# Kernel tuning notes

Measured on AMD Instinct MI355X. Metric: run time of the kernel, lower is better.

## Reference

```python
import jax, jax.numpy as jnp
import numpy as np
from jax import lax

EPS = 1e-5


def _binary(x):
    # binary_tanh / weight binarization with straight-through estimator:
    # forward = sign(x) in {-1,+1}; backward = hard-tanh gradient (pass where |x|<=1)
    hard = jnp.clip(x, -1.0, 1.0)
    sgn = jnp.where(x >= 0, 1.0, -1.0).astype(x.dtype)
    return hard + lax.stop_gradient(sgn - hard)


def _bn2d(x, g, b):
    # training-mode BatchNorm2d over (N,H,W), biased variance (torch semantics)
    m = jnp.mean(x, axis=(0, 2, 3), keepdims=True)
    v = jnp.mean((x - m) ** 2, axis=(0, 2, 3), keepdims=True)
    xn = (x - m) * lax.rsqrt(v + EPS)
    return xn * g[None, :, None, None] + b[None, :, None, None]


def _bn1d(x, g, b):
    m = jnp.mean(x, axis=0, keepdims=True)
    v = jnp.mean((x - m) ** 2, axis=0, keepdims=True)
    return (x - m) * lax.rsqrt(v + EPS) * g[None, :] + b[None, :]


def _conv(x, w, bias):
    y = lax.conv_general_dilated(x, w, window_strides=(1, 1), padding='VALID',
                                 dimension_numbers=('NCHW', 'OIHW', 'NCHW'))
    return y + bias[None, :, None, None]


def _maxpool2(x):
    return lax.reduce_window(x, -jnp.inf, lax.max, (1, 1, 2, 2), (1, 1, 2, 2), 'VALID')


def setup_inputs() -> dict:
    key = jax.random.key(0)
    ks = jax.random.split(key, 16)
    B = 4096
    d = dict(
        x=jax.random.normal(ks[0], (B, 28, 28), jnp.float32),
        conv1_w=jax.random.normal(ks[1], (64, 1, 5, 5), jnp.float32) * 0.05,
        conv1_b=jnp.zeros((64,), jnp.float32),
        bn1_g=jnp.ones((64,), jnp.float32),
        bn1_b=jnp.zeros((64,), jnp.float32),
        conv2_w=jax.random.normal(ks[2], (96, 64, 5, 5), jnp.float32) * 0.05,
        conv2_b=jnp.zeros((96,), jnp.float32),
        bn2_g=jnp.ones((96,), jnp.float32),
        bn2_b=jnp.zeros((96,), jnp.float32),
        bn3_g=jnp.ones((1536,), jnp.float32),
        bn3_b=jnp.zeros((1536,), jnp.float32),
        fc1_w=jax.random.normal(ks[3], (1024, 1536), jnp.float32) * 0.05,
        fc1_b=jnp.zeros((1024,), jnp.float32),
        bn4_g=jnp.ones((1024,), jnp.float32),
        bn4_b=jnp.zeros((1024,), jnp.float32),
        fc2_w=jax.random.normal(ks[4], (10, 1024), jnp.float32) * 0.05,
        fc2_b=jnp.zeros((10,), jnp.float32),
    )
    return d


def reference(x, conv1_w, conv1_b, bn1_g, bn1_b, conv2_w, conv2_b, bn2_g, bn2_b,
              bn3_g, bn3_b, fc1_w, fc1_b, bn4_g, bn4_b, fc2_w, fc2_b):
    h = x[:, None, :, :]                                   # [B,1,28,28]
    h = _maxpool2(_bn2d(_binary(_conv(h, _binary(conv1_w), conv1_b)), bn1_g, bn1_b))  # [B,64,12,12]
    h = _maxpool2(_bn2d(_binary(_conv(h, _binary(conv2_w), conv2_b)), bn2_g, bn2_b))  # [B,96,4,4]
    h = h.reshape(h.shape[0], -1)                          # [B,1536]
    h = _bn1d(h, bn3_g, bn3_b)
    h = _binary(h @ _binary(fc1_w).T + fc1_b[None, :])     # dropout omitted (eval mode)
    h = _bn1d(h, bn4_g, bn4_b)
    return h @ _binary(fc2_w).T + fc2_b[None, :]           # [B,10]
```

## Files before the change

kernel.cpp:

```cpp
#include <hip/hip_runtime.h>
#include <hip/hip_bf16.h>
#include <math.h>


static const double EPSD = 1e-5;
typedef unsigned long long u64;
typedef __attribute__((ext_vector_type(8))) short short8;
typedef __attribute__((ext_vector_type(4))) float floatx4;

#define FIXSCALE 4194304.0

#define O_CNT1   0
#define O_CNT2   256
#define O_CS3    1024
#define O_CS4    7168
#define ZERO_BYTES 11264
#define O_ALPHA1 11264
#define O_BETA1  11776
#define O_ALPHA2 13056
#define O_BETA2  13824
#define O_A3     14592
#define O_B3     26880
#define O_A4     47360
#define O_B4     55552
#define O_C3     63744
#define O_SB     64000
#define O_B1INT  64512
#define O_C2HINT 64768
#define O_W2S    65536
#define O_B3INT  114688
#define O_C1JINT 126976
#define O_S1P    139264
#define O_W1L    139264
#define O_S2BF   15867904
#define O_T4     28450816
#define PLANE    (1024*1536)

__global__ __launch_bounds__(256, 2) void k1_conv1(
    const float* __restrict__ x, const float* __restrict__ w1,
    const float* __restrict__ b1c, const float* __restrict__ g1,
    unsigned short* __restrict__ s1p, unsigned int* __restrict__ cnt1)
{
    __shared__ double X[28*28];
    __shared__ unsigned int redu[256];
    const int b = blockIdx.x;
    const int t = threadIdx.x;
    const float* xb = x + (size_t)b * 784;
    for (int i = t; i < 784; i += 256) X[i] = (double)xb[i];
    const int c = t & 63;
    const int grp = t >> 6;
    double w[25];
#pragma unroll
    for (int k = 0; k < 25; ++k) w[k] = (w1[c*25 + k] >= 0.f) ? 1.0 : -1.0;
    const double bias = (double)b1c[c];
    const bool gpos = (g1[c] >= 0.f);
    __syncthreads();

    unsigned int mycnt = 0;
    for (int pr = grp*3; pr < grp*3 + 3; ++pr) {
        double win[6][6];
#pragma unroll
        for (int r = 0; r < 6; ++r) {
            const double2* p = (const double2*)&X[(2*pr + r)*28];
            double2 a = p[0], bb = p[1], cc = p[2];
            win[r][0]=a.x; win[r][1]=a.y; win[r][2]=bb.x;
            win[r][3]=bb.y; win[r][4]=cc.x; win[r][5]=cc.y;
        }
        unsigned int rowbits = 0;
#pragma unroll
        for (int pc = 0; pc < 12; ++pc) {
            int nplus = 0;
#pragma unroll
            for (int d = 0; d < 4; ++d) {
                const int d0 = d >> 1, d1 = d & 1;
                double acc = 0.0;
#pragma unroll
                for (int ki = 0; ki < 5; ++ki)
#pragma unroll
                    for (int kj = 0; kj < 5; ++kj)
                        acc = fma(w[ki*5 + kj], win[d0 + ki][(2*pc + d1 + kj) % 6], acc);
                acc += bias;
                if (acc >= 0.0) ++nplus;
            }
            mycnt += (unsigned int)nplus;
            const bool s = gpos ? (nplus > 0) : (nplus < 4);
            rowbits |= (s ? 1u : 0u) << pc;
            if (pc < 11) {
#pragma unroll
                for (int r = 0; r < 6; ++r) {
                    const double2 nv = *(const double2*)&X[(2*pr + r)*28 + 2*pc + 6];
                    win[r][(2*pc + 6) % 6] = nv.x;
                    win[r][(2*pc + 7) % 6] = nv.y;
                }
            }
        }
        s1p[((size_t)b*64 + c)*12 + pr] = (unsigned short)rowbits;
    }
    redu[t] = mycnt;
    __syncthreads();
    if (t < 64) {
        unsigned int v = redu[t] + redu[t+64] + redu[t+128] + redu[t+192];
        atomicAdd(&cnt1[t], v);
    }
}

__global__ __launch_bounds__(64) void k2a_consts1(
    const float* __restrict__ g1, const float* __restrict__ b1bn,
    const unsigned int* __restrict__ cnt1,
    double* __restrict__ alpha1, double* __restrict__ beta1,
    unsigned int* __restrict__ B1INT, double* __restrict__ sumBeta)
{
    const int t = threadIdx.x;
    const double N1 = 4096.0 * 576.0;
    double m = (2.0 * (double)cnt1[t] - N1) / N1;
    double r = 1.0 / sqrt((1.0 - m*m) + EPSD);
    double g = (double)g1[t];
    alpha1[t] = (double)b1bn[t] - m * r * g;
    const double bt = fabs(g) * r;
    beta1[t] = bt;
    B1INT[t] = (unsigned int)__double2ll_rn(bt * FIXSCALE);
    double s = bt;
#pragma unroll
    for (int off = 32; off; off >>= 1) s += __shfl_down(s, off);
    if (t == 0) sumBeta[0] = s;
}

__global__ __launch_bounds__(256) void k2b_w2bits(
    const float* __restrict__ w2, u64* __restrict__ W2S)
{
    const int e = blockIdx.x * 256 + threadIdx.x;
    const int o = e >> 6, c = e & 63;
    const float* wp = w2 + (size_t)e * 25;
    unsigned int bits = 0;
#pragma unroll
    for (int k = 0; k < 25; ++k) bits |= (wp[k] >= 0.f ? 1u : 0u) << k;
    const u64 sp = (u64)(bits & 31u)
                 | ((u64)((bits >> 5) & 31u) << 12)
                 | ((u64)((bits >> 10) & 31u) << 24)
                 | ((u64)((bits >> 15) & 31u) << 36)
                 | ((u64)((bits >> 20) & 31u) << 48);
    W2S[c*96 + o] = sp;
}

__global__ __launch_bounds__(64) void k2c_c2(
    const float* __restrict__ w2, const float* __restrict__ b2c,
    const double* __restrict__ alpha1, const double* __restrict__ sumBeta,
    long long* __restrict__ C2HINT)
{
    const int o = blockIdx.x;
    const int c = threadIdx.x;
    const float* wp = w2 + ((size_t)o*64 + c) * 25;
    double sw = 0.0;
#pragma unroll
    for (int k = 0; k < 25; ++k) sw += (wp[k] >= 0.f) ? 1.0 : -1.0;
    double part = sw * alpha1[c];
#pragma unroll
    for (int off = 32; off; off >>= 1) part += __shfl_down(part, off);
    if (c == 0) {
        const double c2h = (part + (double)b2c[o] + 25.0 * sumBeta[0]) * 0.5;
        C2HINT[o] = __double2ll_rn(c2h * FIXSCALE);
    }
}

__global__ __launch_bounds__(384) void k3_conv2(
    const unsigned short* __restrict__ s1p, const u64* __restrict__ W2S,
    const unsigned int* __restrict__ B1INT, const long long* __restrict__ C2HINT,
    const float* __restrict__ g2, unsigned short* __restrict__ s2bf,
    unsigned int* __restrict__ cnt2)
{
    __shared__ unsigned int S32[384];
    __shared__ u64 WB[6144];
    __shared__ unsigned int sBint[64];
    __shared__ unsigned int lcnt[96];
    const int b = blockIdx.x;
    const int t = threadIdx.x;
    const unsigned int* sp32 = (const unsigned int*)(s1p + (size_t)b * 768);
    S32[t] = sp32[t];
    for (int i = t; i < 6144; i += 384) WB[i] = W2S[i];
    if (t < 64) sBint[t] = B1INT[t];
    if (t < 96) lcnt[t] = 0;
    __syncthreads();

    const int o = t % 96;
    const int grp = t / 96;
    const u64 M5 = 0x1FULL | (0x1FULL<<12) | (0x1FULL<<24) | (0x1FULL<<36) | (0x1FULL<<48);
    u64 zm[16];
#pragma unroll
    for (int i = 0; i < 16; ++i) zm[i] = 0ULL;

    for (int c = 0; c < 64; ++c) {
        const u64 wp = WB[c*96 + o];
        const unsigned int d0 = S32[c*6 + grp];
        const unsigned int d1 = S32[c*6 + grp + 1];
        const unsigned int d2 = S32[c*6 + grp + 2];
        const u64 r0 = d0 & 0xFFFFu, r1 = d0 >> 16;
        const u64 r2 = d1 & 0xFFFFu, r3 = d1 >> 16;
        const u64 r4 = d2 & 0xFFFFu, r5 = d2 >> 16;
        const u64 P0 = r0 | (r1 << 12) | (r2 << 24) | (r3 << 36) | (r4 << 48);
        const u64 P1 = (P0 >> 12) | (r5 << 48);
        const u64 Bc = (u64)sBint[c];
#pragma unroll
        for (int j = 0; j < 8; ++j) {
            const u64 m0 = ((P0 >> j) ^ wp) & M5;
            const u64 m1 = ((P1 >> j) ^ wp) & M5;
            zm[j]     += Bc * (u64)(unsigned)__popcll(m0);
            zm[8 + j] += Bc * (u64)(unsigned)__popcll(m1);
        }
    }
    const long long th = C2HINT[o];
    unsigned int tb = 0;
#pragma unroll
    for (int i = 0; i < 16; ++i) tb |= (((long long)zm[i] <= th) ? 1u : 0u) << i;
    atomicAdd(&lcnt[o], (unsigned int)__popc(tb));

    const bool gp = (g2[o] >= 0.f);
    const size_t fbase = (size_t)b*1536 + (size_t)o*16 + (size_t)grp*4;
#pragma unroll
    for (int pj = 0; pj < 4; ++pj) {
        unsigned int four = ((tb >> (2*pj)) & 3u) | (((tb >> (8 + 2*pj)) & 3u) << 2);
        bool s = gp ? (four != 0u) : (four != 15u);
        s2bf[fbase + pj] = s ? (unsigned short)0x3F80 : (unsigned short)0xBF80;
    }
    __syncthreads();
    if (t < 96) atomicAdd(&cnt2[t], lcnt[t]);
}

__global__ __launch_bounds__(128) void k4a_consts2(
    const unsigned int* __restrict__ cnt2, const float* __restrict__ g2,
    const float* __restrict__ b2bn, double* __restrict__ alpha2,
    double* __restrict__ beta2)
{
    const int o = threadIdx.x;
    if (o < 96) {
        const double N2 = 4096.0 * 64.0;
        double m = (2.0 * (double)cnt2[o] - N2) / N2;
        double r = 1.0 / sqrt((1.0 - m*m) + EPSD);
        double g = (double)g2[o];
        alpha2[o] = (double)b2bn[o] - m * r * g;
        beta2[o]  = fabs(g) * r;
    }
}

__global__ __launch_bounds__(192) void k4ba_colsum3(
    const unsigned short* __restrict__ s2bf, int* __restrict__ cs3)
{
    const int t = threadIdx.x;
    const int b0 = blockIdx.x * 128;
    unsigned int a0 = 0, a1 = 0, a2 = 0, a3 = 0;
    for (int k = 0; k < 128; ++k) {
        const uint4 v = *(const uint4*)(s2bf + (size_t)(b0 + k)*1536 + t*8);
        a0 += (v.x >> 15) & 0x00010001u;
        a1 += (v.y >> 15) & 0x00010001u;
        a2 += (v.z >> 15) & 0x00010001u;
        a3 += (v.w >> 15) & 0x00010001u;
    }
    const int base = t * 8;
    atomicAdd(&cs3[base + 0], 128 - 2*(int)(a0 & 0xFFFFu));
    atomicAdd(&cs3[base + 1], 128 - 2*(int)(a0 >> 16));
    atomicAdd(&cs3[base + 2], 128 - 2*(int)(a1 & 0xFFFFu));
    atomicAdd(&cs3[base + 3], 128 - 2*(int)(a1 >> 16));
    atomicAdd(&cs3[base + 4], 128 - 2*(int)(a2 & 0xFFFFu));
    atomicAdd(&cs3[base + 5], 128 - 2*(int)(a2 >> 16));
    atomicAdd(&cs3[base + 6], 128 - 2*(int)(a3 & 0xFFFFu));
    atomicAdd(&cs3[base + 7], 128 - 2*(int)(a3 >> 16));
}

__global__ __launch_bounds__(256) void k4bb_bn3(
    const int* __restrict__ cs3, const double* __restrict__ beta2,
    const float* __restrict__ g3, const float* __restrict__ b3bn,
    double* __restrict__ A3, double* __restrict__ B3, long long* __restrict__ B3INT)
{
    const int f = blockIdx.x * 256 + threadIdx.x;
    const double ms = (double)cs3[f] / 4096.0;
    const int c = f >> 4;
    const double b2v = beta2[c];
    const double var = b2v*b2v*(1.0 - ms*ms);
    const double r = 1.0 / sqrt(var + EPSD);
    const double g = (double)g3[f];
    A3[f] = (double)b3bn[f] - b2v * ms * r * g;
    const double b3v = b2v * r * g;
    B3[f] = b3v;
    B3INT[f] = __double2ll_rn(b3v * FIXSCALE);
}

__global__ __launch_bounds__(256) void k5m_limbs(
    const float* __restrict__ fw1, const long long* __restrict__ B3INT,
    unsigned short* __restrict__ W1L)
{
    const int idx = blockIdx.x * 256 + threadIdx.x;
    const int j = idx / 192, f0 = (idx % 192) * 8;
    const float4 wa = *(const float4*)(fw1 + (size_t)j*1536 + f0);
    const float4 wb = *(const float4*)(fw1 + (size_t)j*1536 + f0 + 4);
    const float wf[8] = {wa.x, wa.y, wa.z, wa.w, wb.x, wb.y, wb.z, wb.w};
    unsigned short ob[5][8];
#pragma unroll
    for (int i = 0; i < 8; ++i) {
        long long xx = B3INT[f0 + i];
        if (wf[i] < 0.f) xx = -xx;
#pragma unroll
        for (int l = 0; l < 5; ++l) {
            const int d = (int)(signed char)(xx & 0xFF);
            xx = (xx - d) >> 8;
            const float fd = (float)d;
            __hip_bfloat16 h = __float2bfloat16(fd);
            ob[l][i] = *(const unsigned short*)&h;
        }
    }
#pragma unroll
    for (int l = 0; l < 5; ++l) {
        uint4 v;
        v.x = (unsigned)ob[l][0] | ((unsigned)ob[l][1] << 16);
        v.y = (unsigned)ob[l][2] | ((unsigned)ob[l][3] << 16);
        v.z = (unsigned)ob[l][4] | ((unsigned)ob[l][5] << 16);
        v.w = (unsigned)ob[l][6] | ((unsigned)ob[l][7] << 16);
        *(uint4*)(W1L + (size_t)l*PLANE + (size_t)j*1536 + f0) = v;
    }
}

__global__ __launch_bounds__(256) void k5_c1j(
    const float* __restrict__ fw1, const float* __restrict__ fc1b,
    const double* __restrict__ A3, long long* __restrict__ c1jint)
{
    const int t = threadIdx.x;
    const int lane = t & 63, w = t >> 6;
    const int j = blockIdx.x * 4 + w;
    double acc = 0.0;
#pragma unroll
    for (int q = 0; q < 6; ++q) {
        const int f0 = q*256 + lane*4;
        const float4 w4 = *(const float4*)(fw1 + (size_t)j*1536 + f0);
        acc += (w4.x >= 0.f) ? A3[f0]   : -A3[f0];
        acc += (w4.y >= 0.f) ? A3[f0+1] : -A3[f0+1];
        acc += (w4.z >= 0.f) ? A3[f0+2] : -A3[f0+2];
        acc += (w4.w >= 0.f) ? A3[f0+3] : -A3[f0+3];
    }
#pragma unroll
    for (int off = 32; off; off >>= 1) acc += __shfl_down(acc, off);
    if (lane == 0) c1jint[j] = __double2ll_rn((acc + (double)fc1b[j]) * FIXSCALE);
}

__global__ __launch_bounds__(512, 2) void k6_fc1(
    const unsigned short* __restrict__ s2bf, const unsigned short* __restrict__ W1L,
    const long long* __restrict__ c1jint, signed char* __restrict__ t4)
{
    __shared__ short sA[128*72];
    __shared__ short sB[5][64*72];
    const int t = threadIdx.x;
    const int b0 = (blockIdx.x & 31) * 128;
    const int j0 = (blockIdx.x >> 5) * 64;
    const int w = t >> 6, lane = t & 63;
    const int wr = w >> 1, wc = w & 1;
    const int l15 = lane & 15, l4 = lane >> 4;

    floatx4 acc[5][2][2];
#pragma unroll
    for (int l5 = 0; l5 < 5; ++l5)
#pragma unroll
        for (int m = 0; m < 2; ++m)
#pragma unroll
            for (int n = 0; n < 2; ++n) acc[l5][m][n] = (floatx4)0.f;

    const int br = t >> 3, bseg = t & 7;
    for (int step = 0; step < 24; ++step) {
        const int k0 = step * 64;
        __syncthreads();
#pragma unroll
        for (int ci = 0; ci < 2; ++ci) {
            const int chunk = t*2 + ci;
            const int ar = chunk >> 3, aseg = chunk & 7;
            const float4 v = *(const float4*)(s2bf + (size_t)(b0+ar)*1536 + k0 + aseg*8);
            *(float4*)(&sA[ar*72 + aseg*8]) = v;
        }
#pragma unroll
        for (int l5 = 0; l5 < 5; ++l5) {
            const float4 v = *(const float4*)(W1L + (size_t)l5*PLANE + (size_t)(j0+br)*1536 + k0 + bseg*8);
            *(float4*)(&sB[l5][br*72 + bseg*8]) = v;
        }
        __syncthreads();
#pragma unroll
        for (int ks = 0; ks < 2; ++ks) {
            short8 a[2];
#pragma unroll
            for (int m = 0; m < 2; ++m)
                a[m] = *(const short8*)(&sA[(wr*32 + m*16 + l15)*72 + ks*32 + l4*8]);
#pragma unroll
            for (int l5 = 0; l5 < 5; ++l5) {
#pragma unroll
                for (int n = 0; n < 2; ++n) {
                    const short8 bfr = *(const short8*)(&sB[l5][(wc*32 + n*16 + l15)*72 + ks*32 + l4*8]);
#pragma unroll
                    for (int m = 0; m < 2; ++m)
                        acc[l5][m][n] = __builtin_amdgcn_mfma_f32_16x16x32_bf16(a[m], bfr, acc[l5][m][n], 0, 0, 0);
                }
            }
        }
    }
#pragma unroll
    for (int n = 0; n < 2; ++n) {
        const int j = j0 + wc*32 + n*16 + l15;
        const long long cj = c1jint[j];
#pragma unroll
        for (int m = 0; m < 2; ++m) {
#pragma unroll
            for (int q = 0; q < 4; ++q) {
                long long z = cj;
#pragma unroll
                for (int l5 = 0; l5 < 5; ++l5)
                    z += ((long long)acc[l5][m][n][q]) << (8*l5);
                const int b = b0 + wr*32 + m*16 + l4*4 + q;
                t4[(size_t)b*1024 + j] = (z >= 0) ? (signed char)1 : (signed char)-1;
            }
        }
    }
}

__global__ __launch_bounds__(256) void k7a_colsum4(
    const signed char* __restrict__ t4, int* __restrict__ cs4)
{
    const int t = threadIdx.x;
    const int seg = t & 63, rowg = t >> 6;
    const int b0 = blockIdx.x * 32;
    unsigned int am0 = 0, am1 = 0, am2 = 0, am3 = 0;
#pragma unroll
    for (int k = 0; k < 8; ++k) {
        const int b = b0 + rowg*8 + k;
        const uint4 v = *(const uint4*)(t4 + (size_t)b*1024 + seg*16);
        am0 += (v.x >> 1) & 0x01010101u;
        am1 += (v.y >> 1) & 0x01010101u;
        am2 += (v.z >> 1) & 0x01010101u;
        am3 += (v.w >> 1) & 0x01010101u;
    }
    __shared__ unsigned int sm[256][4];
    sm[t][0] = am0; sm[t][1] = am1; sm[t][2] = am2; sm[t][3] = am3;
    __syncthreads();
    if (t < 64) {
#pragma unroll
        for (int d = 0; d < 4; ++d) {
            unsigned int m = sm[t][d] + sm[t+64][d] + sm[t+128][d] + sm[t+192][d];
#pragma unroll
            for (int bb = 0; bb < 4; ++bb) {
                int minus = (int)((m >> (8*bb)) & 0xFFu);
                atomicAdd(&cs4[t*16 + d*4 + bb], 32 - 2*minus);
            }
        }
    }
}

__global__ __launch_bounds__(1024) void k7b_bn4(
    const int* __restrict__ cs4, const float* __restrict__ g4,
    const float* __restrict__ b4bn, const float* __restrict__ fc2w,
    const float* __restrict__ fc2b, double* __restrict__ A4,
    double* __restrict__ B4, double* __restrict__ C3)
{
    __shared__ double sA4[1024];
    const int j = threadIdx.x;
    const double m = (double)cs4[j] / 4096.0;
    const double r = 1.0 / sqrt((1.0 - m*m) + EPSD);
    const double g = (double)g4[j];
    const double a4 = (double)b4bn[j] - m * r * g;
    A4[j] = a4;
    B4[j] = r * g;
    sA4[j] = a4;
    __syncthreads();
    if (j < 10) {
        const float* wr = fc2w + (size_t)j * 1024;
        double acc = (double)fc2b[j];
        for (int jj = 0; jj < 1024; ++jj)
            acc += (wr[jj] >= 0.f) ? sA4[jj] : -sA4[jj];
        C3[j] = acc;
    }
}

__global__ __launch_bounds__(256) void k8_fc2(
    const signed char* __restrict__ t4, const float* __restrict__ fc2w,
    const double* __restrict__ B4, const double* __restrict__ C3,
    float* __restrict__ out)
{
    const int t = threadIdx.x;
    const int lane = t & 63;
    const int wv = blockIdx.x * 4 + (t >> 6);
    const int b = wv / 10, kk = wv - b*10;
    const float* wr = fc2w + (size_t)kk * 1024;
    const signed char* tr = t4 + (size_t)b * 1024;
    double acc = 0.0;
#pragma unroll
    for (int q = 0; q < 4; ++q) {
        const int f0 = q*256 + lane*4;
        const float4 w4 = *(const float4*)(wr + f0);
        const unsigned int t4b = *(const unsigned int*)(tr + f0);
        const float wf[4] = {w4.x, w4.y, w4.z, w4.w};
#pragma unroll
        for (int bb = 0; bb < 4; ++bb) {
            const bool ws = (wf[bb] >= 0.f);
            const bool ts = ((t4b >> (8*bb)) & 0x80u) == 0;
            const double bv = B4[f0 + bb];
            acc += (ws == ts) ? bv : -bv;
        }
    }
#pragma unroll
    for (int off = 32; off; off >>= 1) acc += __shfl_down(acc, off);
    if (lane == 0) out[b*10 + kk] = (float)(acc + C3[kk]);
}

extern "C" void kernel_launch(void* const* d_in, const int* in_sizes, int n_in,
                              void* d_out, int out_size, void* d_ws, size_t ws_size,
                              hipStream_t stream)
{
    const float* x    = (const float*)d_in[0];
    const float* w1   = (const float*)d_in[1];
    const float* b1c  = (const float*)d_in[2];
    const float* g1   = (const float*)d_in[3];
    const float* b1bn = (const float*)d_in[4];
    const float* w2   = (const float*)d_in[5];
    const float* b2c  = (const float*)d_in[6];
    const float* g2   = (const float*)d_in[7];
    const float* b2bn = (const float*)d_in[8];
    const float* g3   = (const float*)d_in[9];
    const float* b3bn = (const float*)d_in[10];
    const float* fw1  = (const float*)d_in[11];
    const float* fb1  = (const float*)d_in[12];
    const float* g4   = (const float*)d_in[13];
    const float* b4bn = (const float*)d_in[14];
    const float* fw2  = (const float*)d_in[15];
    const float* fb2  = (const float*)d_in[16];

    char* ws = (char*)d_ws;
    unsigned int* cnt1   = (unsigned int*)(ws + O_CNT1);
    unsigned int* cnt2   = (unsigned int*)(ws + O_CNT2);
    int* cs3             = (int*)(ws + O_CS3);
    int* cs4             = (int*)(ws + O_CS4);
    double* alpha1       = (double*)(ws + O_ALPHA1);
    double* beta1        = (double*)(ws + O_BETA1);
    double* alpha2       = (double*)(ws + O_ALPHA2);
    double* beta2        = (double*)(ws + O_BETA2);
    double* A3           = (double*)(ws + O_A3);
    double* B3           = (double*)(ws + O_B3);
    double* A4           = (double*)(ws + O_A4);
    double* B4           = (double*)(ws + O_B4);
    double* C3           = (double*)(ws + O_C3);
    double* sumBeta      = (double*)(ws + O_SB);
    unsigned int* B1INT  = (unsigned int*)(ws + O_B1INT);
    long long* C2HINT    = (long long*)(ws + O_C2HINT);
    u64* W2S             = (u64*)(ws + O_W2S);
    long long* B3INT     = (long long*)(ws + O_B3INT);
    long long* c1jint    = (long long*)(ws + O_C1JINT);
    unsigned short* s1p  = (unsigned short*)(ws + O_S1P);
    unsigned short* W1L  = (unsigned short*)(ws + O_W1L);
    unsigned short* s2bf = (unsigned short*)(ws + O_S2BF);
    signed char* t4      = (signed char*)(ws + O_T4);

    hipMemsetAsync(ws, 0, ZERO_BYTES, stream);
    k1_conv1<<<4096, 256, 0, stream>>>(x, w1, b1c, g1, s1p, cnt1);
    k2a_consts1<<<1, 64, 0, stream>>>(g1, b1bn, cnt1, alpha1, beta1, B1INT, sumBeta);
    k2b_w2bits<<<24, 256, 0, stream>>>(w2, W2S);
    k2c_c2<<<96, 64, 0, stream>>>(w2, b2c, alpha1, sumBeta, C2HINT);
    k3_conv2<<<4096, 384, 0, stream>>>(s1p, W2S, B1INT, C2HINT, g2, s2bf, cnt2);
    k4a_consts2<<<1, 128, 0, stream>>>(cnt2, g2, b2bn, alpha2, beta2);
    k4ba_colsum3<<<32, 192, 0, stream>>>(s2bf, cs3);
    k4bb_bn3<<<6, 256, 0, stream>>>(cs3, beta2, g3, b3bn, A3, B3, B3INT);
    k5m_limbs<<<768, 256, 0, stream>>>(fw1, B3INT, W1L);
    k5_c1j<<<256, 256, 0, stream>>>(fw1, fb1, A3, c1jint);
    k6_fc1<<<512, 512, 0, stream>>>(s2bf, W1L, c1jint, t4);
    k7a_colsum4<<<128, 256, 0, stream>>>(t4, cs4);
    k7b_bn4<<<1, 1024, 0, stream>>>(cs4, g4, b4bn, fw2, fb2, A4, B4, C3);
    k8_fc2<<<10240, 256, 0, stream>>>(t4, fw2, B4, C3, (float*)d_out);

    (void)in_sizes; (void)n_in; (void)out_size; (void)ws_size;
    (void)beta1; (void)alpha2; (void)B3;
}
```

Measured before the change: 894.1 us.

## Use fp32 conv1 with fp64 fallback near zero; restructure conv2 per output-half

Conv1 now accumulates in fp32 and recomputes in fp64 only when the result lies within 1e-3 of zero, so the sign stays exact while most of the fp64 FMA cost goes away. Conv2 is split into two blocks per image, each covering 48 output channels. The packed row windows are precomputed once into shared memory, and the 64-bit multiply-accumulates are replaced by split 32-bit lo/hi accumulators. Output bf16 values are written as 64-bit words, and the per-channel counts come from a popcount over a shared bit table instead of shared atomics. The fp32 fallback threshold assumes the fp32 rounding error stays below 1e-3.

After: 932.9 us. +4.3%, slower.

```diff
diff --git a/kernel.cpp b/kernel.cpp
--- a/kernel.cpp
+++ b/kernel.cpp
@@ -41,28 +41,29 @@
     const float* __restrict__ b1c, const float* __restrict__ g1,
     unsigned short* __restrict__ s1p, unsigned int* __restrict__ cnt1)
 {
-    __shared__ double X[28*28];
+    __shared__ float X[28*28];
     __shared__ unsigned int redu[256];
     const int b = blockIdx.x;
     const int t = threadIdx.x;
     const float* xb = x + (size_t)b * 784;
-    for (int i = t; i < 784; i += 256) X[i] = (double)xb[i];
+    for (int i = t; i < 784; i += 256) X[i] = xb[i];
     const int c = t & 63;
     const int grp = t >> 6;
-    double w[25];
-#pragma unroll
-    for (int k = 0; k < 25; ++k) w[k] = (w1[c*25 + k] >= 0.f) ? 1.0 : -1.0;
-    const double bias = (double)b1c[c];
+    float w[25];
+#pragma unroll
+    for (int k = 0; k < 25; ++k) w[k] = (w1[c*25 + k] >= 0.f) ? 1.f : -1.f;
+    const float bias = b1c[c];
+    const double biasd = (double)bias;
     const bool gpos = (g1[c] >= 0.f);
     __syncthreads();
 
     unsigned int mycnt = 0;
     for (int pr = grp*3; pr < grp*3 + 3; ++pr) {
-        double win[6][6];
+        float win[6][6];
 #pragma unroll
         for (int r = 0; r < 6; ++r) {
-            const double2* p = (const double2*)&X[(2*pr + r)*28];
-            double2 a = p[0], bb = p[1], cc = p[2];
+            const float2* p = (const float2*)&X[(2*pr + r)*28];
+            float2 a = p[0], bb = p[1], cc = p[2];
             win[r][0]=a.x; win[r][1]=a.y; win[r][2]=bb.x;
             win[r][3]=bb.y; win[r][4]=cc.x; win[r][5]=cc.y;
         }
@@ -73,14 +74,28 @@
 #pragma unroll
             for (int d = 0; d < 4; ++d) {
                 const int d0 = d >> 1, d1 = d & 1;
-                double acc = 0.0;
+                float acc = 0.f;
 #pragma unroll
                 for (int ki = 0; ki < 5; ++ki)
 #pragma unroll
                     for (int kj = 0; kj < 5; ++kj)
-                        acc = fma(w[ki*5 + kj], win[d0 + ki][(2*pc + d1 + kj) % 6], acc);
+                        acc = fmaf(w[ki*5 + kj], win[d0 + ki][(2*pc + d1 + kj) % 6], acc);
                 acc += bias;
-                if (acc >= 0.0) ++nplus;
+                bool pos;
+                if (__builtin_expect(fabsf(acc) < 1e-3f, 0)) {
+                    double ad = 0.0;
+#pragma unroll
+                    for (int ki = 0; ki < 5; ++ki)
+#pragma unroll
+                        for (int kj = 0; kj < 5; ++kj)
+                            ad = fma((double)w[ki*5 + kj],
+                                     (double)win[d0 + ki][(2*pc + d1 + kj) % 6], ad);
+                    ad += biasd;
+                    pos = (ad >= 0.0);
+                } else {
+                    pos = (acc >= 0.f);
+                }
+                nplus += pos ? 1 : 0;
             }
             mycnt += (unsigned int)nplus;
             const bool s = gpos ? (nplus > 0) : (nplus < 4);
@@ -88,7 +103,7 @@
             if (pc < 11) {
 #pragma unroll
                 for (int r = 0; r < 6; ++r) {
-                    const double2 nv = *(const double2*)&X[(2*pr + r)*28 + 2*pc + 6];
+                    const float2 nv = *(const float2*)&X[(2*pr + r)*28 + 2*pc + 6];
                     win[r][(2*pc + 6) % 6] = nv.x;
                     win[r][(2*pc + 7) % 6] = nv.y;
                 }
@@ -169,60 +184,86 @@
     unsigned int* __restrict__ cnt2)
 {
     __shared__ unsigned int S32[384];
-    __shared__ u64 WB[6144];
-    __shared__ unsigned int sBint[64];
-    __shared__ unsigned int lcnt[96];
-    const int b = blockIdx.x;
+    __shared__ u64 WBL[3072];
+    __shared__ u64 PL[512];
+    __shared__ unsigned int sBlo[64], sBhi[64];
+    __shared__ u64 tbitsW[48];
+    const int bid = blockIdx.x;
+    const int b = bid >> 1, ohalf = bid & 1;
     const int t = threadIdx.x;
     const unsigned int* sp32 = (const unsigned int*)(s1p + (size_t)b * 768);
     S32[t] = sp32[t];
-    for (int i = t; i < 6144; i += 384) WB[i] = W2S[i];
-    if (t < 64) sBint[t] = B1INT[t];
-    if (t < 96) lcnt[t] = 0;
+    {
+        const int obase = ohalf * 48;
+#pragma unroll
+        for (int i = t; i < 3072; i += 384) {
+            const int c = i / 48, ol = i - c*48;
+            WBL[i] = W2S[c*96 + obase + ol];
+        }
+    }
+    if (t < 64) { const unsigned int v = B1INT[t]; sBlo[t] = v & 0xFFFFu; sBhi[t] = v >> 16; }
     __syncthreads();
-
-    const int o = t % 96;
-    const int grp = t / 96;
+    for (int idx = t; idx < 512; idx += 384) {
+        const int c = idx >> 3, r = idx & 7;
+        u64 P = 0;
+#pragma unroll
+        for (int i = 0; i < 5; ++i) {
+            const int rr = r + i;
+            const u64 rb = (S32[c*6 + (rr >> 1)] >> (16*(rr & 1))) & 0xFFFFu;
+            P |= rb << (12*i);
+        }
+        PL[idx] = P;
+    }
+    __syncthreads();
+
+    const int ol = t % 48;
+    const int r  = t / 48;
+    const int og = ohalf*48 + ol;
     const u64 M5 = 0x1FULL | (0x1FULL<<12) | (0x1FULL<<24) | (0x1FULL<<36) | (0x1FULL<<48);
-    u64 zm[16];
-#pragma unroll
-    for (int i = 0; i < 16; ++i) zm[i] = 0ULL;
-
+    unsigned int lo[8], hi[8];
+#pragma unroll
+    for (int j = 0; j < 8; ++j) { lo[j] = 0u; hi[j] = 0u; }
+
+#pragma unroll 2
     for (int c = 0; c < 64; ++c) {
-        const u64 wp = WB[c*96 + o];
-        const unsigned int d0 = S32[c*6 + grp];
-        const unsigned int d1 = S32[c*6 + grp + 1];
-        const unsigned int d2 = S32[c*6 + grp + 2];
-        const u64 r0 = d0 & 0xFFFFu, r1 = d0 >> 16;
-        const u64 r2 = d1 & 0xFFFFu, r3 = d1 >> 16;
-        const u64 r4 = d2 & 0xFFFFu, r5 = d2 >> 16;
-        const u64 P0 = r0 | (r1 << 12) | (r2 << 24) | (r3 << 36) | (r4 << 48);
-        const u64 P1 = (P0 >> 12) | (r5 << 48);
-        const u64 Bc = (u64)sBint[c];
+        const u64 wb = WBL[c*48 + ol];
+        u64 X = PL[c*8 + r];
+        const unsigned int bl = sBlo[c], bh = sBhi[c];
 #pragma unroll
         for (int j = 0; j < 8; ++j) {
-            const u64 m0 = ((P0 >> j) ^ wp) & M5;
-            const u64 m1 = ((P1 >> j) ^ wp) & M5;
-            zm[j]     += Bc * (u64)(unsigned)__popcll(m0);
-            zm[8 + j] += Bc * (u64)(unsigned)__popcll(m1);
-        }
-    }
-    const long long th = C2HINT[o];
-    unsigned int tb = 0;
-#pragma unroll
-    for (int i = 0; i < 16; ++i) tb |= (((long long)zm[i] <= th) ? 1u : 0u) << i;
-    atomicAdd(&lcnt[o], (unsigned int)__popc(tb));
-
-    const bool gp = (g2[o] >= 0.f);
-    const size_t fbase = (size_t)b*1536 + (size_t)o*16 + (size_t)grp*4;
-#pragma unroll
-    for (int pj = 0; pj < 4; ++pj) {
-        unsigned int four = ((tb >> (2*pj)) & 3u) | (((tb >> (8 + 2*pj)) & 3u) << 2);
-        bool s = gp ? (four != 0u) : (four != 15u);
-        s2bf[fbase + pj] = s ? (unsigned short)0x3F80 : (unsigned short)0xBF80;
-    }
+            const unsigned int m = (unsigned int)__popcll((X ^ wb) & M5);
+            lo[j] += bl * m;
+            hi[j] += bh * m;
+            X >>= 1;
+        }
+    }
+    const long long th = C2HINT[og];
+    unsigned int tb8 = 0;
+#pragma unroll
+    for (int j = 0; j < 8; ++j) {
+        const long long zm = (long long)lo[j] + ((long long)hi[j] << 16);
+        tb8 |= ((zm <= th) ? 1u : 0u) << j;
+    }
+    ((unsigned char*)tbitsW)[ol*8 + r] = (unsigned char)tb8;
     __syncthreads();
-    if (t < 96) atomicAdd(&cnt2[t], lcnt[t]);
+
+    if (t < 192) {
+        const int po = t >> 2, pr = t & 3;
+        const int oo = ohalf*48 + po;
+        const u64 tw = tbitsW[po];
+        const unsigned int rA = (unsigned int)(tw >> (16*pr)) & 0xFFu;
+        const unsigned int rB = (unsigned int)(tw >> (16*pr + 8)) & 0xFFu;
+        const bool gp = (g2[oo] >= 0.f);
+        u64 word = 0;
+#pragma unroll
+        for (int pj = 0; pj < 4; ++pj) {
+            const unsigned int four = ((rA >> (2*pj)) & 3u) | (((rB >> (2*pj)) & 3u) << 2);
+            const bool s = gp ? (four != 0u) : (four != 15u);
+            word |= (u64)(s ? 0x3F80u : 0xBF80u) << (16*pj);
+        }
+        *(u64*)(s2bf + (size_t)b*1536 + (size_t)oo*16 + pr*4) = word;
+    }
+    if (t < 48) atomicAdd(&cnt2[ohalf*48 + t], (unsigned int)__popcll(tbitsW[t]));
 }
 
 __global__ __launch_bounds__(128) void k4a_consts2(
@@ -554,7 +595,7 @@
     k2a_consts1<<<1, 64, 0, stream>>>(g1, b1bn, cnt1, alpha1, beta1, B1INT, sumBeta);
     k2b_w2bits<<<24, 256, 0, stream>>>(w2, W2S);
     k2c_c2<<<96, 64, 0, stream>>>(w2, b2c, alpha1, sumBeta, C2HINT);
-    k3_conv2<<<4096, 384, 0, stream>>>(s1p, W2S, B1INT, C2HINT, g2, s2bf, cnt2);
+    k3_conv2<<<8192, 384, 0, stream>>>(s1p, W2S, B1INT, C2HINT, g2, s2bf, cnt2);
     k4a_consts2<<<1, 128, 0, stream>>>(cnt2, g2, b2bn, alpha2, beta2);
     k4ba_colsum3<<<32, 192, 0, stream>>>(s2bf, cs3);
     k4bb_bn3<<<6, 256, 0, stream>>>(cs3, beta2, g3, b3bn, A3, B3, B3INT);
```
